# Kernel tuning notes

Measured on AMD Instinct MI355X. Metric: run time of the kernel, lower is better.

## Reference

```python
import jax, jax.numpy as jnp
import numpy as np

B, F, L = 16384, 32, 64
FEAT, DOM, R = 100000, 8, 16
D_IN = F * L  # 2048
N_HIDDEN = 3  # hidden_units = [256, 128, 1]


def _p(k, shape, scale=0.05):
    return jax.random.normal(k, shape, dtype=jnp.float32) * scale


def setup_inputs() -> dict:
    key = jax.random.key(0)
    ks = jax.random.split(key, 32)
    return {
        'x': jax.random.randint(ks[0], (B, F), 0, FEAT),
        'd': jax.random.randint(ks[1], (B,), 0, DOM),
        'emb': _p(ks[2], (FEAT, L)),
        # share MLP: 2048 -> 1024 -> 512 (ReLU after each)
        'sW0': _p(ks[3], (D_IN, 1024)), 'sb0': _p(ks[4], (1024,)),
        'sW1': _p(ks[5], (1024, 512)), 'sb1': _p(ks[6], (512,)),
        # domain layer: 512 -> 256 shared kernel + per-domain LoRA
        'Dk0': _p(ks[7], (512, 256)), 'Db0': _p(ks[8], (256,)),
        'DA0': _p(ks[9], (DOM, 512, R)), 'DB0': _p(ks[10], (DOM, R, 256)), 'Dlb0': _p(ks[11], (DOM, 256)),
        # task layers: 256 -> 128 -> 1 shared kernels + per-task LoRA
        'Tk0': _p(ks[12], (256, 128)), 'Tb0': _p(ks[13], (128,)),
        'Tk1': _p(ks[14], (128, 1)), 'Tb1': _p(ks[15], (1,)),
        'TA0': _p(ks[16], (2, 256, R)), 'TB0': _p(ks[17], (2, R, 128)), 'Tlb0': _p(ks[18], (2, 128)),
        'TA1': _p(ks[19], (2, 128, R)), 'TB1': _p(ks[20], (2, R, 1)), 'Tlb1': _p(ks[21], (2, 1)),
        # gate hypernet + heads
        'gW0': _p(ks[22], (D_IN, 1024)), 'gb0': _p(ks[23], (1024,)),
        'gW1': _p(ks[24], (1024, 512)), 'gb1': _p(ks[25], (512,)),
        'h0W': _p(ks[26], (512, 4)), 'h0b': _p(ks[27], (4,)),
        'h1W': _p(ks[28], (512, 4)), 'h1b': _p(ks[29], (4,)),
    }


def _mlp2(x, W0, b0, W1, b1):
    return jax.nn.relu(jax.nn.relu(x @ W0 + b0) @ W1 + b1)


def _forward(x, d, emb, sW0, sb0, sW1, sb1, Dk0, Db0, DA0, DB0, Dlb0,
             Tk0, Tb0, Tk1, Tb1, TA0, TB0, Tlb0, TA1, TB1, Tlb1,
             gW0, gb0, gW1, gb1, h0W, h0b, h1W, h1b):
    x_emb = emb[x].reshape(x.shape[0], -1)          # (B, dnn_dim)
    x_dnn = _mlp2(x_emb, sW0, sb0, sW1, sb1)        # (B, 512)

    # ---- domain layer (i=0), k=0 -> ReLU applied ----
    share = x_dnn @ Dk0 + Db0                        # (B, 256)
    lora = jnp.einsum('bi,bir->br', x_dnn, DA0[d])   # per-sample domain LoRA gather+matmul
    lora = jnp.einsum('br,bro->bo', lora, DB0[d]) + Dlb0[d]
    d_dnn = jax.nn.relu(share + lora)                # activated
    # d_share / d_lora kept PRE-activation, as in source

    t_dnn = [d_dnn, d_dnn]
    t_share = [share, share]
    t_lora = [lora, lora]
    t_sl, t_ls = [], []
    Tk, Tb = [Tk0, Tk1], [Tb0, Tb1]
    TA, TB, Tlb = [TA0, TA1], [TB0, TB1], [Tlb0, Tlb1]

    k = 1  # shared counter, faithfully incremented per (i, t) step
    for i in range(2):
        for t in range(2):
            ds = t_dnn[t] @ Tk[i] + Tb[i]
            ss = t_share[t] @ Tk[i] + Tb[i]
            ls = t_lora[t] @ Tk[i] + Tb[i]
            t_ls.append(ls)
            A, Bm, lb = TA[i][t], TB[i][t], Tlb[i][t]
            dl = (t_dnn[t] @ A) @ Bm + lb[None, :]
            sl = (t_share[t] @ A) @ Bm + lb[None, :]
            ll = (t_lora[t] @ A) @ Bm + lb[None, :]
            t_dnn[t] = ds + dl
            t_share[t] = ss
            t_lora[t] = ll
            t_sl.append(sl)
            if k + 1 < N_HIDDEN:  # only fires at (i=0, t=0)
                t_dnn[t] = jax.nn.relu(t_dnn[t])
                t_share[t] = jax.nn.relu(t_share[t])
                t_lora[t] = jax.nn.relu(t_lora[t])
                t_sl[t] = jax.nn.relu(t_sl[t])
                t_ls[t] = jax.nn.relu(t_ls[t])
                k += 1

    # ---- gating (hypernet sees detached embedding) ----
    hyper = _mlp2(jax.lax.stop_gradient(x_emb), gW0, gb0, gW1, gb1)
    gates = [jax.nn.sigmoid(hyper @ h0W + h0b), jax.nn.sigmoid(hyper @ h1W + h1b)]

    outs = []
    for t in range(2):
        g = gates[t]
        # t_dnn/t_share/t_lora are (B,1); t_sl[t]/t_ls[t] are (B,128) from i=0 -> broadcast (B,128)
        outs.append(t_dnn[t] - g[:, 0:1] * t_share[t] - g[:, 1:2] * t_lora[t]
                    - g[:, 2:3] * t_sl[t] - g[:, 3:4] * t_ls[t])
    return jnp.stack(outs)  # (2, B, 128)


def reference(x, d, emb, sW0, sb0, sW1, sb1, Dk0, Db0, DA0, DB0, Dlb0,
              Tk0, Tb0, Tk1, Tb1, TA0, TB0, Tlb0, TA1, TB1, Tlb1,
              gW0, gb0, gW1, gb1, h0W, h0b, h1W, h1b):
    return _forward(x, d, emb, sW0, sb0, sW1, sb1, Dk0, Db0, DA0, DB0, Dlb0,
                    Tk0, Tb0, Tk1, Tb1, TA0, TB0, Tlb0, TA1, TB1, Tlb1,
                    gW0, gb0, gW1, gb1, h0W, h0b, h1W, h1b)
```

## Files before the change

kernel.cpp:

```cpp
#include <hip/hip_runtime.h>
#include <hip/hip_bf16.h>

#define BATCH 16384

typedef __attribute__((ext_vector_type(4))) float f32x4;
typedef __attribute__((ext_vector_type(8))) short bf16x8;

__device__ inline float b2f(unsigned short u) {
    union { unsigned u; float f; } c; c.u = ((unsigned)u) << 16; return c.f;
}
__device__ inline unsigned short f2b(float f) {
    __hip_bfloat16 h = __float2bfloat16(f);
    return *(unsigned short*)&h;
}

#define GLL16(g, l)                                                            \
    __builtin_amdgcn_global_load_lds(                                          \
        (const __attribute__((address_space(1))) void*)(g),                    \
        (__attribute__((address_space(3))) void*)(l), 16, 0, 0)

__global__ void k_tcvt2(const float* __restrict__ src0, const float* __restrict__ src1,
                        int K, int N,
                        unsigned short* __restrict__ dst, int off0, int off1, int dst_ld)
{
    __shared__ float t[32][33];
    const float* src = blockIdx.z ? src1 : src0;
    int dst_off = blockIdx.z ? off1 : off0;
    int k0 = blockIdx.y * 32, n0 = blockIdx.x * 32;
    int tx = threadIdx.x, ty = threadIdx.y;
    #pragma unroll
    for (int s = 0; s < 32; s += 8) {
        int k = k0 + ty + s, n = n0 + tx;
        t[ty + s][tx] = (k < K && n < N) ? src[(size_t)k * N + n] : 0.f;
    }
    __syncthreads();
    #pragma unroll
    for (int s = 0; s < 32; s += 8) {
        int n = n0 + ty + s, k = k0 + tx;
        if (n < N && k < K)
            dst[(size_t)(dst_off + n) * dst_ld + k] = f2b(t[tx][ty + s]);
    }
}

__global__ __launch_bounds__(256) void k_smallprep(
    const float* __restrict__ sb0, const float* __restrict__ gb0,
    const float* __restrict__ sb1, const float* __restrict__ gb1,
    const float* __restrict__ Tb0,
    const float* __restrict__ DA0, const float* __restrict__ DB0,
    float* __restrict__ b1cat, float* __restrict__ b2cat, float* __restrict__ tb0c,
    unsigned short* __restrict__ DA0b, unsigned short* __restrict__ DB0b)
{
    int i = blockIdx.x * 256 + threadIdx.x;
    if (i < 1024)            { b1cat[i] = sb0[i]; return; }
    if (i < 2048)            { b1cat[i] = gb0[i - 1024]; return; }
    if (i < 2560)            { b2cat[i - 2048] = sb1[i - 2048]; return; }
    if (i < 3072)            { b2cat[i - 2560 + 512] = gb1[i - 2560]; return; }
    if (i < 3200)            { tb0c[i - 3072] = Tb0[i - 3072]; return; }
    if (i < 3232)            { tb0c[i - 3200 + 128] = 0.f; return; }
    i -= 3232;
    if (i < 65536)           { DA0b[i] = f2b(DA0[i]); return; }
    i -= 65536;
    if (i < 32768)           { DB0b[i] = f2b(DB0[i]); return; }
}

__global__ __launch_bounds__(256) void k_gather(const int* __restrict__ x,
                                                const float* __restrict__ emb,
                                                unsigned short* __restrict__ Xemb)
{
    int i = blockIdx.x * 256 + threadIdx.x;
    int b  = i >> 9;
    int j4 = (i & 511) << 2;
    int f  = j4 >> 6;
    int l  = j4 & 63;
    int idx = x[b * 32 + f];
    float4 v = *(const float4*)(emb + (size_t)idx * 64 + l);
    ushort4 o;
    o.x = f2b(v.x); o.y = f2b(v.y); o.z = f2b(v.z); o.w = f2b(v.w);
    *(ushort4*)(Xemb + (size_t)b * 2048 + j4) = o;
}

template<int RELU, int OUTBF16>
__global__ __launch_bounds__(512, 2) void k_gemm256(
    const unsigned short* __restrict__ A, int lda, long Az,
    const unsigned short* __restrict__ Bt, int K, long Bz,
    const float* __restrict__ bias, int biasz,
    void* __restrict__ C, int ldc, long Cz,
    int N)
{
    extern __shared__ char smem_raw[];
    const int NS = K >> 5;
    const int tid  = threadIdx.x;
    const int lane = tid & 63;
    const int w    = tid >> 6;
    const int wr   = w >> 2, wc = w & 3;
    const int frow = lane & 15, kg = lane >> 4;
    const int z = blockIdx.z;
    A    += (size_t)z * Az;
    Bt   += (size_t)z * Bz;
    bias += (size_t)z * biasz;

    const int gx  = gridDim.x;
    const int nwg = gx * gridDim.y;
    const int lin = blockIdx.y * gx + blockIdx.x;
    const int qq  = nwg >> 3;
    const int swz = (lin & 7) * qq + (lin >> 3);
    const int bx = swz % gx, by = swz / gx;
    const int row0 = by * 256, col0 = bx * 256;

    const int lch = (tid & 7) ^ ((tid >> 3) & 7);
    const unsigned short* gsrc[4];
    int dOff[4];
    #pragma unroll
    for (int h = 0; h < 2; ++h)
        #pragma unroll
        for (int r2 = 0; r2 < 2; ++r2) {
            int rr = h * 128 + r2 * 64 + (tid >> 3);
            const unsigned short* p;
            if (lch < 4) p = A  + (size_t)(row0 + rr) * lda + lch * 8;
            else         p = Bt + (size_t)min(col0 + rr, N - 1) * K + (lch - 4) * 8;
            gsrc[h * 2 + r2] = p;
            dOff[h * 2 + r2] = h * 16384 + r2 * 8192 + w * 1024;
        }

    const int pA = kg ^ (frow & 7);
    const int pB = (4 + kg) ^ (frow & 7);
    int aOff[8], bOff[4];
    #pragma unroll
    for (int m = 0; m < 8; ++m) aOff[m] = (wr * 128 + m * 16 + frow) * 128 + pA * 16;
    #pragma unroll
    for (int n = 0; n < 4; ++n) bOff[n] = (wc * 64 + n * 16 + frow) * 128 + pB * 16;

#define STAGE(sIdx) do {                                                         \
        int rp_ = (sIdx) & 3;                                                    \
        int s_  = min((int)(sIdx), NS - 1);                                      \
        GLL16(gsrc[0] + s_ * 32, smem_raw + rp_ * 32768 + dOff[0]);              \
        GLL16(gsrc[1] + s_ * 32, smem_raw + rp_ * 32768 + dOff[1]);              \
        GLL16(gsrc[2] + s_ * 32, smem_raw + rp_ * 32768 + dOff[2]);              \
        GLL16(gsrc[3] + s_ * 32, smem_raw + rp_ * 32768 + dOff[3]);              \
    } while (0)

    f32x4 acc[8][4] = {};

    STAGE(0); STAGE(1); STAGE(2);
    asm volatile("s_waitcnt vmcnt(8)" ::: "memory");
    __builtin_amdgcn_s_barrier();

    for (int s = 0; s < NS; ++s) {
        const char* sb = smem_raw + (s & 3) * 32768;
        STAGE(s + 3);
        bf16x8 bfr[4], afr[8];
        #pragma unroll
        for (int n = 0; n < 4; ++n) bfr[n] = *(const bf16x8*)(sb + bOff[n]);
        #pragma unroll
        for (int m = 0; m < 8; ++m) afr[m] = *(const bf16x8*)(sb + aOff[m]);
        __builtin_amdgcn_s_setprio(1);
        #pragma unroll
        for (int m = 0; m < 8; ++m)
            #pragma unroll
            for (int n = 0; n < 4; ++n)
                acc[m][n] = __builtin_amdgcn_mfma_f32_16x16x32_bf16(afr[m], bfr[n], acc[m][n], 0, 0, 0);
        __builtin_amdgcn_s_setprio(0);
        asm volatile("s_waitcnt vmcnt(8)" ::: "memory");
        __builtin_amdgcn_s_barrier();
    }
#undef STAGE

    #pragma unroll
    for (int n = 0; n < 4; ++n) {
        int gcol = col0 + wc * 64 + n * 16 + frow;
        if (gcol >= N) continue;
        float bv = bias[gcol];
        #pragma unroll
        for (int m = 0; m < 8; ++m) {
            int gr = row0 + wr * 128 + m * 16 + kg * 4;
            #pragma unroll
            for (int r = 0; r < 4; ++r) {
                float v = acc[m][n][r] + bv;
                if (RELU) v = fmaxf(v, 0.f);
                size_t idx = (size_t)(gr + r) * ldc + gcol;
                if (OUTBF16) ((unsigned short*)C + (size_t)z * Cz)[idx] = f2b(v);
                else         ((float*)C + (size_t)z * Cz)[idx] = v;
            }
        }
    }
}

template<int RELU, int OUTBF16>
__global__ __launch_bounds__(256) void k_gemm(
    const unsigned short* __restrict__ A, int lda,
    const unsigned short* __restrict__ Bt,
    const float* __restrict__ bias,
    void* __restrict__ C, int ldc,
    int N, int K)
{
    __shared__ __align__(16) unsigned short As[128 * 32];
    __shared__ __align__(16) unsigned short Bs[128 * 32];
    const int tid  = threadIdx.x;
    const int lane = tid & 63;
    const int w    = tid >> 6;
    const int wr   = w >> 1, wc = w & 1;
    const int row0 = blockIdx.y * 128;
    const int col0 = blockIdx.x * 128;
    const int frow = lane & 15;
    const int kg   = lane >> 4;
    const int sw   = kg ^ ((frow >> 1) & 3);

    const int srow = w * 32 + (lane >> 2);
    const int csw  = (lane & 3) ^ ((lane >> 3) & 3);
    const int br0  = min(col0 + srow, N - 1);
    const int br1  = min(col0 + srow + 16, N - 1);

    const unsigned short* a0 = A  + (size_t)(row0 + srow) * lda      + csw * 8;
    const unsigned short* a1 = A  + (size_t)(row0 + srow + 16) * lda + csw * 8;
    const unsigned short* b0 = Bt + (size_t)br0 * K + csw * 8;
    const unsigned short* b1 = Bt + (size_t)br1 * K + csw * 8;
    unsigned short* lA0 = As + (w * 2 + 0) * 512;
    unsigned short* lA1 = As + (w * 2 + 1) * 512;
    unsigned short* lB0 = Bs + (w * 2 + 0) * 512;
    unsigned short* lB1 = Bs + (w * 2 + 1) * 512;

    f32x4 acc[4][4] = {};

    for (int bk = 0; bk < K; bk += 32) {
        __syncthreads();
        GLL16(a0 + bk, lA0);
        GLL16(a1 + bk, lA1);
        GLL16(b0 + bk, lB0);
        GLL16(b1 + bk, lB1);
        __syncthreads();
        bf16x8 af[4], bfr[4];
        #pragma unroll
        for (int m = 0; m < 4; ++m)
            af[m] = *(const bf16x8*)&As[(wr * 64 + m * 16 + frow) * 32 + sw * 8];
        #pragma unroll
        for (int n = 0; n < 4; ++n)
            bfr[n] = *(const bf16x8*)&Bs[(wc * 64 + n * 16 + frow) * 32 + sw * 8];
        #pragma unroll
        for (int m = 0; m < 4; ++m)
            #pragma unroll
            for (int n = 0; n < 4; ++n)
                acc[m][n] = __builtin_amdgcn_mfma_f32_16x16x32_bf16(af[m], bfr[n], acc[m][n], 0, 0, 0);
    }

    #pragma unroll
    for (int n = 0; n < 4; ++n) {
        int gcol = col0 + wc * 64 + n * 16 + frow;
        if (gcol >= N) continue;
        float bv = bias[gcol];
        #pragma unroll
        for (int m = 0; m < 4; ++m) {
            int gr = row0 + wr * 64 + m * 16 + kg * 4;
            #pragma unroll
            for (int r = 0; r < 4; ++r) {
                float v = acc[m][n][r] + bv;
                if (RELU) v = fmaxf(v, 0.f);
                size_t idx = (size_t)(gr + r) * ldc + gcol;
                if (OUTBF16) ((unsigned short*)C)[idx] = f2b(v);
                else         ((float*)C)[idx] = v;
            }
        }
    }
}

__global__ __launch_bounds__(256) void k_dlora(
    const unsigned short* __restrict__ Xdnn, const int* __restrict__ d,
    const unsigned short* __restrict__ DA0b, const unsigned short* __restrict__ DB0b,
    const float* __restrict__ Dlb0,
    const unsigned short* __restrict__ SHARE,
    unsigned short* __restrict__ LORA, unsigned short* __restrict__ DDNN)
{
    int w = threadIdx.x >> 6, lane = threadIdx.x & 63;
    int b = blockIdx.x * 4 + w;
    int dom = d[b];
    uint4 raw = *(const uint4*)(Xdnn + (size_t)b * 512 + lane * 8);
    const unsigned short* pr = (const unsigned short*)&raw;
    float xv[8];
    #pragma unroll
    for (int j = 0; j < 8; ++j) xv[j] = b2f(pr[j]);

    const unsigned short* Ap = DA0b + ((size_t)dom * 512 + lane * 8) * 16;
    float v[16];
    #pragma unroll
    for (int r = 0; r < 16; ++r) v[r] = 0.f;
    #pragma unroll
    for (int j = 0; j < 8; ++j) {
        uint4 a0 = *(const uint4*)(Ap + j * 16);
        uint4 a1 = *(const uint4*)(Ap + j * 16 + 8);
        const unsigned short* ap = (const unsigned short*)&a0;
        const unsigned short* aq = (const unsigned short*)&a1;
        float xj = xv[j];
        #pragma unroll
        for (int r = 0; r < 8; ++r) v[r]     += xj * b2f(ap[r]);
        #pragma unroll
        for (int r = 0; r < 8; ++r) v[r + 8] += xj * b2f(aq[r]);
    }
    #pragma unroll
    for (int s = 1; s < 64; s <<= 1) {
        #pragma unroll
        for (int r = 0; r < 16; ++r) v[r] += __shfl_xor(v[r], s, 64);
    }
    const unsigned short* Bp = DB0b + (size_t)dom * 16 * 256;
    const float* lbp = Dlb0 + (size_t)dom * 256;
    #pragma unroll
    for (int c = 0; c < 4; ++c) {
        int o = lane + c * 64;
        float a = lbp[o];
        #pragma unroll
        for (int r = 0; r < 16; ++r) a += v[r] * b2f(Bp[r * 256 + o]);
        float sh = b2f(SHARE[(size_t)b * 256 + o]);
        LORA[(size_t)b * 256 + o] = f2b(a);
        DDNN[(size_t)b * 256 + o] = f2b(fmaxf(sh + a, 0.f));
    }
}

__global__ __launch_bounds__(256) void k_tail(
    const float* __restrict__ Yd, const float* __restrict__ Ys, const float* __restrict__ Yl,
    const unsigned short* __restrict__ Hyper,
    const float* __restrict__ TB0, const float* __restrict__ Tlb0,
    const float* __restrict__ Tk1, const float* __restrict__ Tb1,
    const float* __restrict__ TA1, const float* __restrict__ TB1, const float* __restrict__ Tlb1,
    const float* __restrict__ h0W, const float* __restrict__ h0b,
    const float* __restrict__ h1W, const float* __restrict__ h1b,
    float* __restrict__ out)
{
    __shared__ float sTB0[2][16][128];
    __shared__ float sTlb0[2][128];
    __shared__ float sTk1[128];
    __shared__ float sWeff[2][128];
    __shared__ float sY[4][3][160];
    const int tid = threadIdx.x;

    for (int i = tid; i < 4096; i += 256) ((float*)sTB0)[i] = TB0[i];
    if (tid < 256) ((float*)sTlb0)[tid] = Tlb0[tid];
    if (tid < 128) sTk1[tid] = Tk1[tid];
    {
        int t = tid >> 7, j = tid & 127;
        float a = 0.f;
        #pragma unroll
        for (int r = 0; r < 16; ++r) a += TA1[((size_t)t * 128 + j) * 16 + r] * TB1[t * 16 + r];
        sWeff[t][j] = a;
    }
    const float* Yp[3] = {Yd, Ys, Yl};
    int b0 = blockIdx.x * 4;
    for (int i = tid; i < 4 * 3 * 160; i += 256) {
        int s = i / 480, rem = i % 480, st = rem / 160, idx = rem % 160;
        sY[s][st][idx] = Yp[st][(size_t)(b0 + s) * 160 + idx];
    }
    __syncthreads();

    int w = tid >> 6, lane = tid & 63;
    int b = b0 + w;
    const float* yd = sY[w][0];
    const float* ys = sY[w][1];
    const float* yl = sY[w][2];
    int j0 = lane, j1 = lane + 64;

    uint4 hraw = *(const uint4*)(Hyper + (size_t)b * 512 + lane * 8);
    const unsigned short* hp = (const unsigned short*)&hraw;
    float hv[8];
    #pragma unroll
    for (int j = 0; j < 8; ++j) hv[j] = b2f(hp[j]);

    float red[14];
    #pragma unroll
    for (int k = 0; k < 14; ++k) red[k] = 0.f;
    #pragma unroll
    for (int j = 0; j < 8; ++j) {
        float4 w0 = *(const float4*)(h0W + (size_t)(lane * 8 + j) * 4);
        float4 w1 = *(const float4*)(h1W + (size_t)(lane * 8 + j) * 4);
        red[0] += hv[j] * w0.x; red[1] += hv[j] * w0.y; red[2] += hv[j] * w0.z; red[3] += hv[j] * w0.w;
        red[4] += hv[j] * w1.x; red[5] += hv[j] * w1.y; red[6] += hv[j] * w1.z; red[7] += hv[j] * w1.w;
    }

    float SLv[2][2], LSv[2][2];
    #pragma unroll
    for (int t = 0; t < 2; ++t) {
        float lb0 = sTlb0[t][j0], lb1 = sTlb0[t][j1];
        float dl0 = lb0, dl1 = lb1, sl0 = lb0, sl1 = lb1, ll0 = lb0, ll1 = lb1;
        #pragma unroll
        for (int r = 0; r < 16; ++r) {
            float w0v = sTB0[t][r][j0], w1v = sTB0[t][r][j1];
            float ud = yd[128 + t * 16 + r];
            float us = ys[128 + t * 16 + r];
            float ul = yl[128 + t * 16 + r];
            dl0 += ud * w0v; dl1 += ud * w1v;
            sl0 += us * w0v; sl1 += us * w1v;
            ll0 += ul * w0v; ll1 += ul * w1v;
        }
        float D0 = yd[j0] + dl0, D1 = yd[j1] + dl1;
        float S0 = ys[j0],       S1 = ys[j1];
        float L0 = ll0,          L1 = ll1;
        float sl_0 = sl0, sl_1 = sl1;
        float ls_0 = yl[j0], ls_1 = yl[j1];
        if (t == 0) {
            D0 = fmaxf(D0, 0.f); D1 = fmaxf(D1, 0.f);
            S0 = fmaxf(S0, 0.f); S1 = fmaxf(S1, 0.f);
            L0 = fmaxf(L0, 0.f); L1 = fmaxf(L1, 0.f);
            sl_0 = fmaxf(sl_0, 0.f); sl_1 = fmaxf(sl_1, 0.f);
            ls_0 = fmaxf(ls_0, 0.f); ls_1 = fmaxf(ls_1, 0.f);
        }
        SLv[t][0] = sl_0; SLv[t][1] = sl_1;
        LSv[t][0] = ls_0; LSv[t][1] = ls_1;
        float we0 = sWeff[t][j0], we1 = sWeff[t][j1];
        float tk0 = sTk1[j0],     tk1v = sTk1[j1];
        red[8 + t * 3 + 0] = D0 * (tk0 + we0) + D1 * (tk1v + we1);
        red[8 + t * 3 + 1] = S0 * tk0 + S1 * tk1v;
        red[8 + t * 3 + 2] = L0 * we0 + L1 * we1;
    }

    #pragma unroll
    for (int s = 1; s < 64; s <<= 1) {
        #pragma unroll
        for (int k = 0; k < 14; ++k) red[k] += __shfl_xor(red[k], s, 64);
    }

    float Tb1v = Tb1[0];
    #pragma unroll
    for (int t = 0; t < 2; ++t) {
        float fd = red[8 + t * 3 + 0] + Tb1v + Tlb1[t];
        float fs = red[8 + t * 3 + 1] + Tb1v;
        float fl = red[8 + t * 3 + 2] + Tlb1[t];
        const float* hb = t ? h1b : h0b;
        float g0 = 1.f / (1.f + expf(-(red[t * 4 + 0] + hb[0])));
        float g1 = 1.f / (1.f + expf(-(red[t * 4 + 1] + hb[1])));
        float g2 = 1.f / (1.f + expf(-(red[t * 4 + 2] + hb[2])));
        float g3 = 1.f / (1.f + expf(-(red[t * 4 + 3] + hb[3])));
        float base = fd - g0 * fs - g1 * fl;
        size_t o = (size_t)t * BATCH * 128 + (size_t)b * 128;
        out[o + j0] = base - g2 * SLv[t][0] - g3 * LSv[t][0];
        out[o + j1] = base - g2 * SLv[t][1] - g3 * LSv[t][1];
    }
}

extern "C" void kernel_launch(void* const* d_in, const int* in_sizes, int n_in,
                              void* d_out, int out_size, void* d_ws, size_t ws_size,
                              hipStream_t stream)
{
    const int*   x    = (const int*)  d_in[0];
    const int*   dix  = (const int*)  d_in[1];
    const float* emb  = (const float*)d_in[2];
    const float* sW0  = (const float*)d_in[3];
    const float* sb0  = (const float*)d_in[4];
    const float* sW1  = (const float*)d_in[5];
    const float* sb1  = (const float*)d_in[6];
    const float* Dk0  = (const float*)d_in[7];
    const float* Db0  = (const float*)d_in[8];
    const float* DA0  = (const float*)d_in[9];
    const float* DB0  = (const float*)d_in[10];
    const float* Dlb0 = (const float*)d_in[11];
    const float* Tk0  = (const float*)d_in[12];
    const float* Tb0  = (const float*)d_in[13];
    const float* Tk1  = (const float*)d_in[14];
    const float* Tb1  = (const float*)d_in[15];
    const float* TA0  = (const float*)d_in[16];
    const float* TB0  = (const float*)d_in[17];
    const float* Tlb0 = (const float*)d_in[18];
    const float* TA1  = (const float*)d_in[19];
    const float* TB1  = (const float*)d_in[20];
    const float* Tlb1 = (const float*)d_in[21];
    const float* gW0  = (const float*)d_in[22];
    const float* gb0  = (const float*)d_in[23];
    const float* gW1  = (const float*)d_in[24];
    const float* gb1  = (const float*)d_in[25];
    const float* h0W  = (const float*)d_in[26];
    const float* h0b  = (const float*)d_in[27];
    const float* h1W  = (const float*)d_in[28];
    const float* h1b  = (const float*)d_in[29];

    hipFuncSetAttribute((const void*)k_gemm256<1, 1>,
                        hipFuncAttributeMaxDynamicSharedMemorySize, 131072);

    char* ws = (char*)d_ws;
    size_t off = 0;
    auto alloc = [&](size_t bytes) -> void* {
        void* p = ws + off;
        off += (bytes + 255) & ~(size_t)255;
        return p;
    };
    unsigned short* W1t   = (unsigned short*)alloc((size_t)2048 * 2048 * 2);
    unsigned short* W2cat = (unsigned short*)alloc((size_t)1024 * 1024 * 2);
    unsigned short* Dk0t  = (unsigned short*)alloc((size_t)256 * 512 * 2);
    unsigned short* Tcat  = (unsigned short*)alloc((size_t)160 * 256 * 2);
    unsigned short* DA0b  = (unsigned short*)alloc((size_t)8 * 512 * 16 * 2);
    unsigned short* DB0b  = (unsigned short*)alloc((size_t)8 * 16 * 256 * 2);
    float*          b1cat = (float*)alloc(2048 * 4);
    float*          b2cat = (float*)alloc(1024 * 4);
    float*          tb0c  = (float*)alloc(160 * 4);
    char* regA = (char*)alloc((size_t)BATCH * 2048 * 2);
    char* regB = (char*)alloc((size_t)BATCH * 2048 * 2);
    unsigned short* Xdnn  = (unsigned short*)alloc((size_t)BATCH * 512 * 2);
    unsigned short* Hyper = (unsigned short*)alloc((size_t)BATCH * 512 * 2);

    unsigned short* Xemb = (unsigned short*)regA;
    float* Ybase = (float*)regA;
    float* Ys = Ybase;
    float* Yl = Ybase + (size_t)BATCH * 160;
    float* Yd = Ybase + (size_t)2 * BATCH * 160;
    unsigned short* Hbuf  = (unsigned short*)regB;
    unsigned short* SHARE = (unsigned short*)regB;
    unsigned short* LORA  = SHARE + (size_t)BATCH * 256;
    unsigned short* DDNN  = LORA  + (size_t)BATCH * 256;

    dim3 tb(32, 8);
    k_tcvt2<<<dim3(32, 64, 2), tb, 0, stream>>>(sW0, gW0, 2048, 1024, W1t, 0, 1024, 2048);
    k_tcvt2<<<dim3(16, 32, 2), tb, 0, stream>>>(sW1, gW1, 1024, 512, W2cat, 0, 512, 1024);
    k_tcvt2<<<dim3(8, 16, 1),  tb, 0, stream>>>(Dk0, Dk0, 512, 256, Dk0t, 0, 0, 512);
    k_tcvt2<<<dim3(4, 8, 1),   tb, 0, stream>>>(Tk0, Tk0, 256, 128, Tcat, 0, 0, 256);
    k_tcvt2<<<dim3(1, 8, 2),   tb, 0, stream>>>(TA0, TA0 + 256 * 16, 256, 16, Tcat, 128, 144, 256);
    k_smallprep<<<397, 256, 0, stream>>>(sb0, gb0, sb1, gb1, Tb0, DA0, DB0,
                                         b1cat, b2cat, tb0c, DA0b, DB0b);

    k_gather<<<32768, 256, 0, stream>>>(x, emb, Xemb);
    k_gemm256<1, 1><<<dim3(8, 64, 1), 512, 131072, stream>>>(
        Xemb, 2048, 0, W1t, 2048, 0, b1cat, 0, Hbuf, 2048, 0, 2048);
    k_gemm256<1, 1><<<dim3(2, 64, 2), 512, 131072, stream>>>(
        Hbuf, 2048, 1024, W2cat, 1024, (long)512 * 1024, b2cat, 512,
        Xdnn, 512, (long)BATCH * 512, 512);
    k_gemm<0, 1><<<dim3(2, 128), 256, 0, stream>>>(Xdnn, 512, Dk0t, Db0, SHARE, 256, 256, 512);
    k_dlora<<<BATCH / 4, 256, 0, stream>>>(Xdnn, dix, DA0b, DB0b, Dlb0, SHARE, LORA, DDNN);
    k_gemm<0, 0><<<dim3(2, 384), 256, 0, stream>>>(SHARE, 256, Tcat, tb0c, Ybase, 160, 160, 256);
    k_tail<<<BATCH / 4, 256, 0, stream>>>(Yd, Ys, Yl, Hyper, TB0, Tlb0, Tk1, Tb1,
                                          TA1, TB1, Tlb1, h0W, h0b, h1W, h1b, (float*)d_out);
}
```

Before: 374.6 us.

## Restructure 256x256 GEMM mainloop into ping-pong K=64 double-buffer with vectorized epilogue

Rewrites the large GEMM kernel's main loop to stage 64-wide K tiles into two 64KB slots. Each tile is split into two 32-wide halves, and each half's MFMA work is split into two 16-instruction groups. Explicit barriers and lgkm/vm waits interleave LDS reads, global-to-LDS prefetch and MFMA so memory and compute overlap, similar to a ping-pong schedule. Both GEMM kernels swap the MFMA operands so each lane holds four consecutive output columns, which allows float4 bias loads and ushort4/float4 stores in the epilogue. The 256 kernel drops the N bounds check, and the extra barriers could add sync overhead.

```diff
diff --git a/kernel.cpp b/kernel.cpp
--- a/kernel.cpp
+++ b/kernel.cpp
@@ -88,7 +88,7 @@
     int N)
 {
     extern __shared__ char smem_raw[];
-    const int NS = K >> 5;
+    const int NT = K >> 6;
     const int tid  = threadIdx.x;
     const int lane = tid & 63;
     const int w    = tid >> 6;
@@ -107,79 +107,103 @@
     const int bx = swz % gx, by = swz / gx;
     const int row0 = by * 256, col0 = bx * 256;
 
-    const int lch = (tid & 7) ^ ((tid >> 3) & 7);
+    const int lch = (lane & 7) ^ ((lane >> 3) & 7);
     const unsigned short* gsrc[4];
-    int dOff[4];
-    #pragma unroll
-    for (int h = 0; h < 2; ++h)
-        #pragma unroll
-        for (int r2 = 0; r2 < 2; ++r2) {
-            int rr = h * 128 + r2 * 64 + (tid >> 3);
-            const unsigned short* p;
-            if (lch < 4) p = A  + (size_t)(row0 + rr) * lda + lch * 8;
-            else         p = Bt + (size_t)min(col0 + rr, N - 1) * K + (lch - 4) * 8;
-            gsrc[h * 2 + r2] = p;
-            dOff[h * 2 + r2] = h * 16384 + r2 * 8192 + w * 1024;
-        }
-
-    const int pA = kg ^ (frow & 7);
-    const int pB = (4 + kg) ^ (frow & 7);
+    #pragma unroll
+    for (int h = 0; h < 4; ++h) {
+        int rr = h * 64 + w * 8 + (lane >> 3);
+        if (lch < 4) gsrc[h] = A  + (size_t)(row0 + rr) * lda + lch * 8;
+        else         gsrc[h] = Bt + (size_t)min(col0 + rr, N - 1) * K + (lch - 4) * 8;
+    }
+    const int dBase = w * 1024;
+
+    const int pA = (kg ^ (frow & 7)) * 16;
+    const int pB = ((4 + kg) ^ (frow & 7)) * 16;
     int aOff[8], bOff[4];
     #pragma unroll
-    for (int m = 0; m < 8; ++m) aOff[m] = (wr * 128 + m * 16 + frow) * 128 + pA * 16;
-    #pragma unroll
-    for (int n = 0; n < 4; ++n) bOff[n] = (wc * 64 + n * 16 + frow) * 128 + pB * 16;
-
-#define STAGE(sIdx) do {                                                         \
-        int rp_ = (sIdx) & 3;                                                    \
-        int s_  = min((int)(sIdx), NS - 1);                                      \
-        GLL16(gsrc[0] + s_ * 32, smem_raw + rp_ * 32768 + dOff[0]);              \
-        GLL16(gsrc[1] + s_ * 32, smem_raw + rp_ * 32768 + dOff[1]);              \
-        GLL16(gsrc[2] + s_ * 32, smem_raw + rp_ * 32768 + dOff[2]);              \
-        GLL16(gsrc[3] + s_ * 32, smem_raw + rp_ * 32768 + dOff[3]);              \
+    for (int m = 0; m < 8; ++m) aOff[m] = (wr * 128 + m * 16 + frow) * 128 + pA;
+    #pragma unroll
+    for (int n = 0; n < 4; ++n) bOff[n] = (wc * 64 + n * 16 + frow) * 128 + pB;
+
+#define STAGE(t_, ks_, slot_) do {                                               \
+        int s_ = min((int)(t_), NT - 1) * 64 + (ks_) * 32;                       \
+        char* d_ = smem_raw + (slot_) * 65536 + (ks_) * 32768 + dBase;           \
+        GLL16(gsrc[0] + s_, d_);                                                 \
+        GLL16(gsrc[1] + s_, d_ + 8192);                                          \
+        GLL16(gsrc[2] + s_, d_ + 16384);                                         \
+        GLL16(gsrc[3] + s_, d_ + 24576);                                         \
     } while (0)
+#define READS_B(sb_, ks_)                                                        \
+        _Pragma("unroll")                                                        \
+        for (int n = 0; n < 4; ++n)                                              \
+            bfr[n] = *(const bf16x8*)(smem_raw + (sb_) + (ks_) * 32768 + bOff[n]);
+#define READS_A(sb_, ks_, mh_)                                                   \
+        _Pragma("unroll")                                                        \
+        for (int mi = 0; mi < 4; ++mi)                                           \
+            afr[mi] = *(const bf16x8*)(smem_raw + (sb_) + (ks_) * 32768 + aOff[(mh_) * 4 + mi]);
+#define MFMA16(mh_) do {                                                         \
+        __builtin_amdgcn_s_setprio(1);                                           \
+        _Pragma("unroll")                                                        \
+        for (int mi = 0; mi < 4; ++mi)                                           \
+            _Pragma("unroll")                                                    \
+            for (int n = 0; n < 4; ++n)                                          \
+                acc[(mh_) * 4 + mi][n] = __builtin_amdgcn_mfma_f32_16x16x32_bf16( \
+                    bfr[n], afr[mi], acc[(mh_) * 4 + mi][n], 0, 0, 0);           \
+        __builtin_amdgcn_s_setprio(0);                                           \
+    } while (0)
+#define LGKM0 asm volatile("s_waitcnt lgkmcnt(0)" ::: "memory")
+#define VM4   asm volatile("s_waitcnt vmcnt(4)" ::: "memory")
+#define BAR   __builtin_amdgcn_s_barrier()
 
     f32x4 acc[8][4] = {};
-
-    STAGE(0); STAGE(1); STAGE(2);
-    asm volatile("s_waitcnt vmcnt(8)" ::: "memory");
-    __builtin_amdgcn_s_barrier();
-
-    for (int s = 0; s < NS; ++s) {
-        const char* sb = smem_raw + (s & 3) * 32768;
-        STAGE(s + 3);
-        bf16x8 bfr[4], afr[8];
-        #pragma unroll
-        for (int n = 0; n < 4; ++n) bfr[n] = *(const bf16x8*)(sb + bOff[n]);
-        #pragma unroll
-        for (int m = 0; m < 8; ++m) afr[m] = *(const bf16x8*)(sb + aOff[m]);
-        __builtin_amdgcn_s_setprio(1);
-        #pragma unroll
-        for (int m = 0; m < 8; ++m)
-            #pragma unroll
-            for (int n = 0; n < 4; ++n)
-                acc[m][n] = __builtin_amdgcn_mfma_f32_16x16x32_bf16(afr[m], bfr[n], acc[m][n], 0, 0, 0);
-        __builtin_amdgcn_s_setprio(0);
-        asm volatile("s_waitcnt vmcnt(8)" ::: "memory");
-        __builtin_amdgcn_s_barrier();
+    bf16x8 afr[4], bfr[4];
+
+    STAGE(0, 0, 0); STAGE(0, 1, 0);
+    VM4; BAR;
+
+    for (int t = 0; t < NT; ++t) {
+        const int slot = t & 1, nslot = slot ^ 1;
+        const int sb = slot * 65536;
+        READS_B(sb, 0); READS_A(sb, 0, 0);
+        STAGE(t + 1, 0, nslot);
+        BAR; LGKM0; MFMA16(0); BAR;
+        READS_A(sb, 0, 1);
+        VM4;
+        BAR; LGKM0; MFMA16(1); BAR;
+        READS_B(sb, 1); READS_A(sb, 1, 0);
+        STAGE(t + 1, 1, nslot);
+        BAR; LGKM0; MFMA16(0); BAR;
+        READS_A(sb, 1, 1);
+        VM4;
+        BAR; LGKM0; MFMA16(1); BAR;
     }
 #undef STAGE
-
-    #pragma unroll
-    for (int n = 0; n < 4; ++n) {
-        int gcol = col0 + wc * 64 + n * 16 + frow;
-        if (gcol >= N) continue;
-        float bv = bias[gcol];
-        #pragma unroll
-        for (int m = 0; m < 8; ++m) {
-            int gr = row0 + wr * 128 + m * 16 + kg * 4;
-            #pragma unroll
-            for (int r = 0; r < 4; ++r) {
-                float v = acc[m][n][r] + bv;
-                if (RELU) v = fmaxf(v, 0.f);
-                size_t idx = (size_t)(gr + r) * ldc + gcol;
-                if (OUTBF16) ((unsigned short*)C + (size_t)z * Cz)[idx] = f2b(v);
-                else         ((float*)C + (size_t)z * Cz)[idx] = v;
+#undef READS_B
+#undef READS_A
+#undef MFMA16
+#undef LGKM0
+#undef VM4
+#undef BAR
+
+    #pragma unroll
+    for (int m = 0; m < 8; ++m) {
+        int row = row0 + wr * 128 + m * 16 + frow;
+        #pragma unroll
+        for (int n = 0; n < 4; ++n) {
+            int col = col0 + wc * 64 + n * 16 + kg * 4;
+            float4 bv = *(const float4*)(bias + col);
+            float v0 = acc[m][n][0] + bv.x, v1 = acc[m][n][1] + bv.y;
+            float v2 = acc[m][n][2] + bv.z, v3 = acc[m][n][3] + bv.w;
+            if (RELU) {
+                v0 = fmaxf(v0, 0.f); v1 = fmaxf(v1, 0.f);
+                v2 = fmaxf(v2, 0.f); v3 = fmaxf(v3, 0.f);
+            }
+            if (OUTBF16) {
+                ushort4 o = { f2b(v0), f2b(v1), f2b(v2), f2b(v3) };
+                *(ushort4*)((unsigned short*)C + (size_t)z * Cz + (size_t)row * ldc + col) = o;
+            } else {
+                float4 o = { v0, v1, v2, v3 };
+                *(float4*)((float*)C + (size_t)z * Cz + (size_t)row * ldc + col) = o;
             }
         }
     }
@@ -239,24 +263,29 @@
         for (int m = 0; m < 4; ++m)
             #pragma unroll
             for (int n = 0; n < 4; ++n)
-                acc[m][n] = __builtin_amdgcn_mfma_f32_16x16x32_bf16(af[m], bfr[n], acc[m][n], 0, 0, 0);
-    }
-
-    #pragma unroll
-    for (int n = 0; n < 4; ++n) {
-        int gcol = col0 + wc * 64 + n * 16 + frow;
-        if (gcol >= N) continue;
-        float bv = bias[gcol];
-        #pragma unroll
-        for (int m = 0; m < 4; ++m) {
-            int gr = row0 + wr * 64 + m * 16 + kg * 4;
-            #pragma unroll
-            for (int r = 0; r < 4; ++r) {
-                float v = acc[m][n][r] + bv;
-                if (RELU) v = fmaxf(v, 0.f);
-                size_t idx = (size_t)(gr + r) * ldc + gcol;
-                if (OUTBF16) ((unsigned short*)C)[idx] = f2b(v);
-                else         ((float*)C)[idx] = v;
+                acc[m][n] = __builtin_amdgcn_mfma_f32_16x16x32_bf16(bfr[n], af[m], acc[m][n], 0, 0, 0);
+    }
+
+    #pragma unroll
+    for (int m = 0; m < 4; ++m) {
+        int row = row0 + wr * 64 + m * 16 + frow;
+        #pragma unroll
+        for (int n = 0; n < 4; ++n) {
+            int col = col0 + wc * 64 + n * 16 + kg * 4;
+            if (col >= N) continue;
+            float4 bv = *(const float4*)(bias + col);
+            float v0 = acc[m][n][0] + bv.x, v1 = acc[m][n][1] + bv.y;
+            float v2 = acc[m][n][2] + bv.z, v3 = acc[m][n][3] + bv.w;
+            if (RELU) {
+                v0 = fmaxf(v0, 0.f); v1 = fmaxf(v1, 0.f);
+                v2 = fmaxf(v2, 0.f); v3 = fmaxf(v3, 0.f);
+            }
+            if (OUTBF16) {
+                ushort4 o = { f2b(v0), f2b(v1), f2b(v2), f2b(v3) };
+                *(ushort4*)((unsigned short*)C + (size_t)row * ldc + col) = o;
+            } else {
+                float4 o = { v0, v1, v2, v3 };
+                *(float4*)((float*)C + (size_t)row * ldc + col) = o;
             }
         }
     }
```

Measured after the change: 378.7 us. No clear change (+1.1%).
